# Performance work log

Measured on AMD Instinct MI355X. Metric: run time of the kernel, lower is better.

Reference implementation:

```python
import jax, jax.numpy as jnp
import numpy as np
from jax import lax


def setup_inputs() -> dict:
    key = jax.random.key(0)
    kx, kk = jax.random.split(key)
    B, H, W, Cin, Cout, K = 32, 128, 128, 128, 128, 3
    X = jax.random.normal(kx, (B, H, W, Cin), dtype=jnp.float32)
    kernel = jax.random.normal(kk, (B, K, K, Cin, Cout), dtype=jnp.float32)
    return {"X": X, "kernel": kernel}


def reference(X, kernel):
    """Per-sample dynamic conv2d: each batch element gets its own HWIO kernel.

    Equivalent math to the TF depthwise-trick + reduce_sum, but expressed as a
    vmapped standard convolution (fuses the input-channel reduction, avoiding
    the huge [H',W',B*Cin,Cout] intermediate). Padding = 'VALID'.
    """
    dn = ('NHWC', 'HWIO', 'NHWC')

    def conv_one(x, k):
        # x: [H, W, Cin], k: [kh, kw, Cin, Cout] -> [H', W', Cout]
        return lax.conv_general_dilated(
            x[None], k, window_strides=(1, 1), padding='VALID',
            dimension_numbers=dn)[0]

    return jax.vmap(conv_one)(X, kernel)  # [B, H', W', Cout]
```

## Files before the change

kernel.cpp:

```cpp
#include <hip/hip_runtime.h>
#include <stdint.h>

typedef __attribute__((ext_vector_type(8))) short bf16x8;
typedef __attribute__((ext_vector_type(4))) float f32x4;
typedef __attribute__((ext_vector_type(4))) unsigned short u16x4;

#define NB 32
#define HH 128
#define WW 128
#define CI 128
#define CO 128
#define HO 126
#define WO 126
#define TH 16
#define TW 16
#define PHh 18
#define PWw 18

__device__ __forceinline__ unsigned short f2bf(float f) {
  union { float f; unsigned u; } x; x.f = f;
  unsigned u = x.u;
  u += 0x7FFFu + ((u >> 16) & 1u);
  return (unsigned short)(u >> 16);
}

__device__ __forceinline__ int swz64(int idx) { return idx ^ (((idx >> 6) & 7) << 3); }

__global__ void prep_kt(const float* __restrict__ kin, unsigned short* __restrict__ ktr) {
  __shared__ unsigned short t[CI * CO];
  int bp = blockIdx.x;
  int b = bp / 9, p = bp % 9;
  const float* src = kin + (size_t)bp * (CI * CO);
  unsigned short* dstb = ktr + (size_t)b * (9 * CI * CO);
  for (int i = threadIdx.x; i < CI * CO / 4; i += blockDim.x) {
    f32x4 v = *(const f32x4*)(src + i * 4);
    u16x4 o;
    o.x = f2bf(v.x); o.y = f2bf(v.y); o.z = f2bf(v.z); o.w = f2bf(v.w);
    *(u16x4*)&t[i * 4] = o;
  }
  __syncthreads();
  for (int j = threadIdx.x; j < 2048; j += blockDim.x) {
    int lane = j & 63, f = (j >> 6) & 7, sl = j >> 9;
    int ch = sl >> 1, kc = sl & 1;
    int co = (f >> 2) * 64 + (f & 3) * 16 + (lane & 15);
    int ci0 = ch * 64 + kc * 32 + (lane >> 4) * 8;
    bf16x8 v;
#pragma unroll
    for (int e = 0; e < 8; ++e) v[e] = t[(ci0 + e) * CO + co];
    int slice = (ch * 9 + p) * 2 + kc;
    *(bf16x8*)&dstb[(size_t)slice * 4096 + f * 512 + lane * 8] = v;
  }
}

__global__ void conv_naive(const float* __restrict__ X, const float* __restrict__ Kf,
                           float* __restrict__ out) {
  int idx = blockIdx.x * blockDim.x + threadIdx.x;
  if (idx >= NB * HO * WO * CO) return;
  int co = idx & 127, t = idx >> 7;
  int wp = t % WO; t /= WO;
  int hp = t % HO; int b = t / HO;
  const float* xb = X + (size_t)b * HH * WW * CI;
  const float* kb = Kf + (size_t)b * 9 * CI * CO;
  float s = 0.f;
  for (int p = 0; p < 9; ++p) {
    int kh = p / 3, kw = p % 3;
    const float* xr = xb + ((size_t)(hp + kh) * WW + (wp + kw)) * CI;
    const float* kr = kb + (size_t)p * CI * CO + co;
    for (int ci = 0; ci < CI; ++ci) s += xr[ci] * kr[(size_t)ci * CO];
  }
  out[idx] = s;
}

__global__ __launch_bounds__(512, 4) void conv_main(
    const float* __restrict__ X, const unsigned short* __restrict__ Kt,
    float* __restrict__ out) {
  __shared__ unsigned short lds_a[PHh * PWw * 64];

  const int tid = threadIdx.x;
  const int lane = tid & 63;
  const int wid = tid >> 6;
  const int wr = wid >> 1, wc = wid & 1;

  const int l = blockIdx.x;
  const int xcd = l & 7, j = l >> 3;
  const int b = xcd * 4 + (j >> 6);
  const int t = j & 63;
  const int ht = t >> 3, wt = t & 7;
  const int h0 = ht * TH, w0 = wt * TW;
  const int ks = lane >> 4, lr = lane & 15;

  const float* xb = X + (size_t)b * HH * WW * CI;

  auto stageA = [&](int ch) {
    for (int s = tid; s < PHh * PWw * 16; s += 512) {
      int ci4 = s & 15;
      int row = s >> 4;
      int w = row % PWw;
      int h = row / PWw;
      int gh = h0 + h, gw = w0 + w;
      f32x4 v = {0.f, 0.f, 0.f, 0.f};
      if (gh < HH && gw < WW)
        v = *(const f32x4*)(xb + ((size_t)(gh * WW + gw)) * CI + ch * 64 + ci4 * 4);
      u16x4 o;
      o.x = f2bf(v.x); o.y = f2bf(v.y); o.z = f2bf(v.z); o.w = f2bf(v.w);
      *(u16x4*)&lds_a[swz64(row * 64 + ci4 * 4)] = o;
    }
  };

  f32x4 zero = {0.f, 0.f, 0.f, 0.f};
  f32x4 acc[4][4];
#pragma unroll
  for (int m = 0; m < 4; ++m)
#pragma unroll
    for (int n = 0; n < 4; ++n) acc[m][n] = zero;

  const unsigned short* ktw = Kt + (size_t)b * 9 * CI * CO + (wc * 4) * 512 + lane * 8;

  bf16x8 H[4];
  auto loadBh = [&](int slice) {
#pragma unroll
    for (int n = 0; n < 4; ++n)
      H[n] = *(const bf16x8*)&ktw[(size_t)slice * 4096 + n * 512];
  };

  auto comph = [&](int s) {
    int p = s >> 1, kc = s & 1;
    int kh = p < 3 ? 0 : (p < 6 ? 1 : 2);
    int kw = p - kh * 3;
    bf16x8 af[4];
#pragma unroll
    for (int m = 0; m < 4; ++m) {
      int row = (wr * 4 + m + kh) * PWw + lr + kw;
      af[m] = *(const bf16x8*)&lds_a[swz64(row * 64 + kc * 32 + ks * 8)];
    }
    __builtin_amdgcn_s_setprio(1);
#pragma unroll
    for (int m = 0; m < 4; ++m)
#pragma unroll
      for (int n = 0; n < 4; ++n)
        acc[m][n] = __builtin_amdgcn_mfma_f32_16x16x32_bf16(af[m], H[n], acc[m][n], 0, 0, 0);
    __builtin_amdgcn_s_setprio(0);
  };

#pragma unroll 1
  for (int ch = 0; ch < 2; ++ch) {
    if (ch) __syncthreads();
    stageA(ch);
    loadBh(ch * 18);
    __syncthreads();
#pragma unroll 1
    for (int s = 0; s < 18; ++s) {
      comph(s);
      if (s + 1 < 18) loadBh(ch * 18 + s + 1);
    }
  }

  float* ob = out + (size_t)b * HO * WO * CO;
#pragma unroll
  for (int m = 0; m < 4; ++m) {
    int hp = h0 + wr * 4 + m;
    if (hp >= HO) continue;
#pragma unroll
    for (int r = 0; r < 4; ++r) {
      int wp = w0 + ks * 4 + r;
      if (wp >= WO) continue;
#pragma unroll
      for (int n = 0; n < 4; ++n) {
        int co = wc * 64 + n * 16 + lr;
        ob[((size_t)hp * WO + wp) * CO + co] = acc[m][n][r];
      }
    }
  }
}

extern "C" void kernel_launch(void* const* d_in, const int* in_sizes, int n_in,
                              void* d_out, int out_size, void* d_ws, size_t ws_size,
                              hipStream_t stream) {
  const float* X = (const float*)d_in[0];
  const float* Kf = (const float*)d_in[1];
  float* out = (float*)d_out;
  size_t need = (size_t)NB * 9 * CI * CO * sizeof(unsigned short);
  if (d_ws != nullptr && ws_size >= need) {
    unsigned short* ktr = (unsigned short*)d_ws;
    prep_kt<<<dim3(NB * 9), 256, 0, stream>>>(Kf, ktr);
    conv_main<<<dim3(2048), 512, 0, stream>>>(X, ktr, out);
  } else {
    int total = NB * HO * WO * CO;
    conv_naive<<<(total + 255) / 256, 256, 0, stream>>>(X, Kf, out);
  }
}
```

Measured before the change: 206.9 us.

## Double-buffer input tile in LDS across 32-channel chunks with overlapped staging

Splits the input-channel reduction into four 32-channel chunks held in two LDS buffers, so global loads of the next chunk are issued during the MFMA work on the current one and written to the other buffer after a few taps. This is meant to hide global-load and staging latency and to remove the extra barrier per 64-channel chunk. It also switches to a padded row stride of 40 in place of the XOR swizzle, uses the hardware packed bf16 convert instruction, and precomputes staging addresses. The cost is more LDS per block, which may affect occupancy, and more live registers from the in-flight loads.

```diff
diff --git a/kernel.cpp b/kernel.cpp
--- a/kernel.cpp
+++ b/kernel.cpp
@@ -4,6 +4,7 @@
 typedef __attribute__((ext_vector_type(8))) short bf16x8;
 typedef __attribute__((ext_vector_type(4))) float f32x4;
 typedef __attribute__((ext_vector_type(4))) unsigned short u16x4;
+typedef __attribute__((ext_vector_type(4))) unsigned int u32x4;
 
 #define NB 32
 #define HH 128
@@ -16,6 +17,9 @@
 #define TW 16
 #define PHh 18
 #define PWw 18
+#define NROW (PHh * PWw)
+#define RSTR 40
+#define QBUF (NROW * RSTR)
 
 __device__ __forceinline__ unsigned short f2bf(float f) {
   union { float f; unsigned u; } x; x.f = f;
@@ -24,7 +28,11 @@
   return (unsigned short)(u >> 16);
 }
 
-__device__ __forceinline__ int swz64(int idx) { return idx ^ (((idx >> 6) & 7) << 3); }
+__device__ __forceinline__ unsigned cvtpk_bf16(float a, float b) {
+  unsigned r;
+  asm("v_cvt_pk_bf16_f32 %0, %1, %2" : "=v"(r) : "v"(a), "v"(b));
+  return r;
+}
 
 __global__ void prep_kt(const float* __restrict__ kin, unsigned short* __restrict__ ktr) {
   __shared__ unsigned short t[CI * CO];
@@ -74,7 +82,7 @@
 __global__ __launch_bounds__(512, 4) void conv_main(
     const float* __restrict__ X, const unsigned short* __restrict__ Kt,
     float* __restrict__ out) {
-  __shared__ unsigned short lds_a[PHh * PWw * 64];
+  __shared__ unsigned short lds_a[2][QBUF];
 
   const int tid = threadIdx.x;
   const int lane = tid & 63;
@@ -91,68 +99,114 @@
 
   const float* xb = X + (size_t)b * HH * WW * CI;
 
-  auto stageA = [&](int ch) {
-    for (int s = tid; s < PHh * PWw * 16; s += 512) {
-      int ci4 = s & 15;
-      int row = s >> 4;
-      int w = row % PWw;
-      int h = row / PWw;
-      int gh = h0 + h, gw = w0 + w;
-      f32x4 v = {0.f, 0.f, 0.f, 0.f};
-      if (gh < HH && gw < WW)
-        v = *(const f32x4*)(xb + ((size_t)(gh * WW + gw)) * CI + ch * 64 + ci4 * 4);
-      u16x4 o;
-      o.x = f2bf(v.x); o.y = f2bf(v.y); o.z = f2bf(v.z); o.w = f2bf(v.w);
-      *(u16x4*)&lds_a[swz64(row * 64 + ci4 * 4)] = o;
+  int sdst[3]; const float* ssrc[3]; bool sz[3];
+#pragma unroll
+  for (int i = 0; i < 3; ++i) {
+    int s = tid + i * 512;
+    int row = s >> 2, g = s & 3;
+    int h = row / PWw, w = row - h * PWw;
+    int gh = h0 + h, gw = w0 + w;
+    sdst[i] = (s < NROW * 4) ? (row * RSTR + g * 8) : -1;
+    sz[i] = (gh >= HH) | (gw >= WW);
+    ssrc[i] = xb + ((size_t)((gh & 127) * WW + (gw & 127))) * CI + g * 8;
+  }
+
+  int aoff[4];
+#pragma unroll
+  for (int m = 0; m < 4; ++m)
+    aoff[m] = ((wr * 4 + m) * PWw + lr) * RSTR + ks * 8;
+
+  const unsigned short* ktw = Kt + (size_t)b * 9 * CI * CO + (wc * 4) * 512 + lane * 8;
+
+  const f32x4 zero4 = {0.f, 0.f, 0.f, 0.f};
+
+  auto sissue = [&](int i, int q, f32x4& lo, f32x4& hi) {
+    lo = zero4; hi = zero4;
+    if (sdst[i] >= 0 && !sz[i]) {
+      const float* p = ssrc[i] + q * 32;
+      lo = *(const f32x4*)p;
+      hi = *(const f32x4*)(p + 4);
     }
   };
-
-  f32x4 zero = {0.f, 0.f, 0.f, 0.f};
+  auto swrite = [&](int i, unsigned short* wb, const f32x4& lo, const f32x4& hi) {
+    if (sdst[i] >= 0) {
+      u32x4 r;
+      r.x = cvtpk_bf16(lo.x, lo.y);
+      r.y = cvtpk_bf16(lo.z, lo.w);
+      r.z = cvtpk_bf16(hi.x, hi.y);
+      r.w = cvtpk_bf16(hi.z, hi.w);
+      *(u32x4*)&wb[sdst[i]] = r;
+    }
+  };
+
+  bf16x8 Hf[4];
+  auto loadB = [&](const unsigned short* p) {
+#pragma unroll
+    for (int n = 0; n < 4; ++n)
+      Hf[n] = *(const bf16x8*)(p + n * 512);
+  };
+
+  {
+    f32x4 al, ah, bl, bh;
+    sissue(0, 0, al, ah);
+    sissue(1, 0, bl, bh);
+    loadB(ktw);
+    swrite(0, lds_a[0], al, ah);
+    sissue(2, 0, al, ah);
+    swrite(1, lds_a[0], bl, bh);
+    swrite(2, lds_a[0], al, ah);
+  }
+  __syncthreads();
+
   f32x4 acc[4][4];
 #pragma unroll
   for (int m = 0; m < 4; ++m)
 #pragma unroll
-    for (int n = 0; n < 4; ++n) acc[m][n] = zero;
-
-  const unsigned short* ktw = Kt + (size_t)b * 9 * CI * CO + (wc * 4) * 512 + lane * 8;
-
-  bf16x8 H[4];
-  auto loadBh = [&](int slice) {
-#pragma unroll
-    for (int n = 0; n < 4; ++n)
-      H[n] = *(const bf16x8*)&ktw[(size_t)slice * 4096 + n * 512];
-  };
-
-  auto comph = [&](int s) {
-    int p = s >> 1, kc = s & 1;
-    int kh = p < 3 ? 0 : (p < 6 ? 1 : 2);
-    int kw = p - kh * 3;
-    bf16x8 af[4];
-#pragma unroll
-    for (int m = 0; m < 4; ++m) {
-      int row = (wr * 4 + m + kh) * PWw + lr + kw;
-      af[m] = *(const bf16x8*)&lds_a[swz64(row * 64 + kc * 32 + ks * 8)];
-    }
-    __builtin_amdgcn_s_setprio(1);
-#pragma unroll
-    for (int m = 0; m < 4; ++m)
-#pragma unroll
-      for (int n = 0; n < 4; ++n)
-        acc[m][n] = __builtin_amdgcn_mfma_f32_16x16x32_bf16(af[m], H[n], acc[m][n], 0, 0, 0);
-    __builtin_amdgcn_s_setprio(0);
-  };
+    for (int n = 0; n < 4; ++n) acc[m][n] = zero4;
+
+  f32x4 glo, ghi;
+  const unsigned short* bptr = ktw;
 
 #pragma unroll 1
-  for (int ch = 0; ch < 2; ++ch) {
-    if (ch) __syncthreads();
-    stageA(ch);
-    loadBh(ch * 18);
-    __syncthreads();
-#pragma unroll 1
-    for (int s = 0; s < 18; ++s) {
-      comph(s);
-      if (s + 1 < 18) loadBh(ch * 18 + s + 1);
-    }
+  for (int q = 0; q < 4; ++q) {
+    const unsigned short* rb = lds_a[q & 1];
+    unsigned short* wb = lds_a[(q & 1) ^ 1];
+    const bool st = (q < 3);
+#pragma unroll
+    for (int p = 0; p < 9; ++p) {
+      const int kh = p / 3, kw = p % 3;
+      const int dp = (kh * PWw + kw) * RSTR;
+      if (st && p == 0) sissue(0, q + 1, glo, ghi);
+      if (st && p == 3) sissue(1, q + 1, glo, ghi);
+      if (st && p == 6) sissue(2, q + 1, glo, ghi);
+
+      bf16x8 af[4];
+#pragma unroll
+      for (int m = 0; m < 4; ++m)
+        af[m] = *(const bf16x8*)&rb[aoff[m] + dp];
+
+      __builtin_amdgcn_s_setprio(1);
+#pragma unroll
+      for (int m = 0; m < 4; ++m)
+#pragma unroll
+        for (int n = 0; n < 4; ++n)
+          acc[m][n] = __builtin_amdgcn_mfma_f32_16x16x32_bf16(af[m], Hf[n], acc[m][n], 0, 0, 0);
+      __builtin_amdgcn_s_setprio(0);
+
+      if (p < 8) {
+        bptr += 8192;
+        loadB(bptr);
+      } else if (q < 3) {
+        int q2 = q + 1;
+        bptr = ktw + (size_t)((q2 >> 1) * 18 + (q2 & 1)) * 4096;
+        loadB(bptr);
+      }
+
+      if (st && p == 2) swrite(0, wb, glo, ghi);
+      if (st && p == 5) swrite(1, wb, glo, ghi);
+      if (st && p == 8) swrite(2, wb, glo, ghi);
+    }
+    if (q < 3) __syncthreads();
   }
 
   float* ob = out + (size_t)b * HO * WO * CO;
```

After: 424.1 us. 2.05x slower.

## Halve conv tile height to 256-thread blocks and batch staging loads in flight

Applied to the files above, without the earlier changes.

The output tile shrinks from 16x16 to 8x16 pixels, and blocks go from 512 to 256 threads, so the grid doubles to 4096 blocks. The input-staging loop is rewritten to keep four global float4 loads in flight before converting to bf16 and writing to LDS. The aim is better occupancy and load balance across CUs, plus hiding global-load latency during staging. In exchange, the halo overhead per tile rises (10x18 staged rows for 8x16 outputs) and each weight slice is fetched by twice as many blocks.

```diff
diff --git a/kernel.cpp b/kernel.cpp
--- a/kernel.cpp
+++ b/kernel.cpp
@@ -12,10 +12,12 @@
 #define CO 128
 #define HO 126
 #define WO 126
-#define TH 16
+#define TH 8
 #define TW 16
-#define PHh 18
+#define PHh 10
 #define PWw 18
+#define NROW (PHh * PWw)
+#define NSLOT (NROW * 16)
 
 __device__ __forceinline__ unsigned short f2bf(float f) {
   union { float f; unsigned u; } x; x.f = f;
@@ -71,10 +73,10 @@
   out[idx] = s;
 }
 
-__global__ __launch_bounds__(512, 4) void conv_main(
+__global__ __launch_bounds__(256, 4) void conv_main(
     const float* __restrict__ X, const unsigned short* __restrict__ Kt,
     float* __restrict__ out) {
-  __shared__ unsigned short lds_a[PHh * PWw * 64];
+  __shared__ unsigned short lds_a[NROW * 64];
 
   const int tid = threadIdx.x;
   const int lane = tid & 63;
@@ -83,27 +85,41 @@
 
   const int l = blockIdx.x;
   const int xcd = l & 7, j = l >> 3;
-  const int b = xcd * 4 + (j >> 6);
-  const int t = j & 63;
+  const int b = xcd * 4 + (j >> 7);
+  const int t = j & 127;
   const int ht = t >> 3, wt = t & 7;
   const int h0 = ht * TH, w0 = wt * TW;
   const int ks = lane >> 4, lr = lane & 15;
 
   const float* xb = X + (size_t)b * HH * WW * CI;
 
-  auto stageA = [&](int ch) {
-    for (int s = tid; s < PHh * PWw * 16; s += 512) {
-      int ci4 = s & 15;
-      int row = s >> 4;
-      int w = row % PWw;
-      int h = row / PWw;
-      int gh = h0 + h, gw = w0 + w;
-      f32x4 v = {0.f, 0.f, 0.f, 0.f};
-      if (gh < HH && gw < WW)
-        v = *(const f32x4*)(xb + ((size_t)(gh * WW + gw)) * CI + ch * 64 + ci4 * 4);
+  f32x4 sv[4]; int sdd[4];
+  auto sissue = [&](int k, int jj, int ch) {
+    int s = tid + (k << 8);
+    bool valid = s < NSLOT;
+    int ci4 = s & 15, row = s >> 4;
+    int h = row / PWw, w = row - h * PWw;
+    int gh = h0 + h, gw = w0 + w;
+    f32x4 v = {0.f, 0.f, 0.f, 0.f};
+    if (valid && gh < HH && gw < WW)
+      v = *(const f32x4*)(xb + ((size_t)(gh * WW + gw)) * CI + ch * 64 + ci4 * 4);
+    sv[jj] = v;
+    sdd[jj] = valid ? swz64(row * 64 + ci4 * 4) : -1;
+  };
+  auto swrite = [&](int jj) {
+    if (sdd[jj] >= 0) {
+      f32x4 v = sv[jj];
       u16x4 o;
       o.x = f2bf(v.x); o.y = f2bf(v.y); o.z = f2bf(v.z); o.w = f2bf(v.w);
-      *(u16x4*)&lds_a[swz64(row * 64 + ci4 * 4)] = o;
+      *(u16x4*)&lds_a[sdd[jj]] = o;
+    }
+  };
+  auto stageA = [&](int ch) {
+    sissue(0, 0, ch); sissue(1, 1, ch); sissue(2, 2, ch); sissue(3, 3, ch);
+#pragma unroll
+    for (int k = 0; k < 12; ++k) {
+      swrite(k & 3);
+      if (k + 4 < 12) sissue(k + 4, (k + 4) & 3, ch);
     }
   };
 
@@ -116,11 +132,11 @@
 
   const unsigned short* ktw = Kt + (size_t)b * 9 * CI * CO + (wc * 4) * 512 + lane * 8;
 
-  bf16x8 H[4];
+  bf16x8 Hf[4];
   auto loadBh = [&](int slice) {
 #pragma unroll
     for (int n = 0; n < 4; ++n)
-      H[n] = *(const bf16x8*)&ktw[(size_t)slice * 4096 + n * 512];
+      Hf[n] = *(const bf16x8*)&ktw[(size_t)slice * 4096 + n * 512];
   };
 
   auto comph = [&](int s) {
@@ -138,7 +154,7 @@
     for (int m = 0; m < 4; ++m)
 #pragma unroll
       for (int n = 0; n < 4; ++n)
-        acc[m][n] = __builtin_amdgcn_mfma_f32_16x16x32_bf16(af[m], H[n], acc[m][n], 0, 0, 0);
+        acc[m][n] = __builtin_amdgcn_mfma_f32_16x16x32_bf16(af[m], Hf[n], acc[m][n], 0, 0, 0);
     __builtin_amdgcn_s_setprio(0);
   };
 
@@ -183,7 +199,7 @@
   if (d_ws != nullptr && ws_size >= need) {
     unsigned short* ktr = (unsigned short*)d_ws;
     prep_kt<<<dim3(NB * 9), 256, 0, stream>>>(Kf, ktr);
-    conv_main<<<dim3(2048), 512, 0, stream>>>(X, ktr, out);
+    conv_main<<<dim3(4096), 256, 0, stream>>>(X, ktr, out);
   } else {
     int total = NB * HO * WO * CO;
     conv_naive<<<(total + 255) / 256, 256, 0, stream>>>(X, Kf, out);
```

Measured after the change: 250.6 us. 1.21x slower.
